# Kernel optimization log

Hardware: AMD Instinct MI355X
Metric: run time of the kernel (lower is better)

## Reference

```python
import jax, jax.numpy as jnp
import numpy as np

NU = 256      # numunits
NH = 32       # torch.split chunk size == head dim in this code
B = 128
S = 256


def _linear_tanh(x, W, b):
    # torch nn.Linear: y = x @ W.T + b, followed by tanh
    return jnp.tanh(x @ W.T + b)


def _split_heads(x):
    # torch.split(x, NH, dim=-1) then cat(dim=0): chunk c occupies rows [c*B, (c+1)*B)
    b, s, d = x.shape
    c = d // NH
    return x.reshape(b, s, c, NH).transpose(2, 0, 1, 3).reshape(c * b, s, NH)


def _merge_heads(x, b):
    # torch.split(x, batchsize, dim=0) then cat(dim=-1): inverse of _split_heads
    cb, s, hd = x.shape
    c = cb // b
    return x.reshape(c, b, s, hd).transpose(1, 2, 0, 3).reshape(b, s, c * hd)


def _attention(Q, K, V):
    d_k = jnp.asarray(K.shape[2], Q.dtype) ** 0.5
    scores = jnp.einsum('nqd,nkd->nqk', Q, K) / d_k
    # NB: original uses F.softmax(scores) with no dim on a 3D tensor ->
    # torch legacy default is dim=0. We reproduce that exactly.
    p_attn = jax.nn.softmax(scores, axis=0)
    return jnp.einsum('nqk,nkd->nqd', p_attn, V)


def setup_inputs() -> dict:
    key = jax.random.key(0)
    ks = jax.random.split(key, 24)
    def w(k):
        return jax.random.normal(k, (NU, NU), dtype=jnp.float32) * 0.02
    def bvec(k):
        return jax.random.normal(k, (NU,), dtype=jnp.float32) * 0.02
    inp = {
        'queries1': jax.random.normal(ks[0], (B, S, NU), dtype=jnp.float32),
        'queries2': jax.random.normal(ks[1], (B, S, NU), dtype=jnp.float32),
        'queries3': jax.random.normal(ks[2], (B, S, NU), dtype=jnp.float32),
        'adj': jax.random.randint(ks[3], (B,), 0, B, dtype=jnp.int64),
        'WQ': w(ks[4]),  'bQ': bvec(ks[5]),
        'WV': w(ks[6]),  'bV': bvec(ks[7]),
        'WQ3': w(ks[8]), 'bQ3': bvec(ks[9]),
        'WK3': w(ks[10]), 'bK3': bvec(ks[11]),
        'WV3': w(ks[12]), 'bV3': bvec(ks[13]),
        'WQ4': w(ks[14]), 'bQ4': bvec(ks[15]),
        'WV4': w(ks[16]), 'bV4': bvec(ks[17]),
        'W5': jax.random.normal(ks[18], (NU, 4 * NU), dtype=jnp.float32) * 0.02,
        'b5': bvec(ks[19]),
    }
    return inp


def reference(queries1, queries2, queries3, adj,
              WQ, bQ, WV, bV, WQ3, bQ3, WK3, bK3, WV3, bV3,
              WQ4, bQ4, WV4, bV4, W5, b5):
    b = queries1.shape[0]
    # per-row batch gather: queries4[i] = queries3[adj[i]]
    queries4 = queries3[adj]

    Q1 = _split_heads(_linear_tanh(queries1, WQ, bQ))
    Q2 = _split_heads(_linear_tanh(queries2, WQ, bQ))
    Q3 = _split_heads(_linear_tanh(queries3, WQ3, bQ3))
    Q4 = _split_heads(_linear_tanh(queries4, WQ4, bQ4))
    K3 = _split_heads(_linear_tanh(queries3, WK3, bK3))
    V1 = _split_heads(_linear_tanh(queries1, WV, bV))
    V2 = _split_heads(_linear_tanh(queries2, WV, bV))
    V3 = _split_heads(_linear_tanh(queries3, WV3, bV3))
    V4 = _split_heads(_linear_tanh(queries4, WV4, bV4))

    o1 = _merge_heads(_attention(Q1, K3, V1), b)
    o2 = _merge_heads(_attention(Q2, K3, V2), b)
    o3 = _merge_heads(_attention(Q3, K3, V3), b)
    o4 = _merge_heads(_attention(Q4, K3, V4), b)

    o5 = jnp.tanh(jnp.concatenate([o1, o2, o3, o4], axis=-1) @ W5.T + b5)
    return (o1, o2, o5, o3)
```

## Files before the change

### kernel.cpp

```cpp
#include <hip/hip_runtime.h>


typedef __attribute__((ext_vector_type(4))) float f32x4;
typedef __attribute__((ext_vector_type(8))) short bf16x8;

#define LOG2E 1.4426950408889634f
#define SM_SCALE (1.4426950408889634f / 5.656854249492381f)

#define CVT_PK(d, lo, hi) \
    asm("v_cvt_pk_bf16_f32 %0, %1, %2" : "=v"(d) : "v"(lo), "v"(hi))
#define SWAP32(x, y) \
    asm("v_permlane32_swap_b32 %0, %1" : "+v"(x), "+v"(y))
#define SWAP16(x, y) \
    asm("v_permlane16_swap_b32 %0, %1" : "+v"(x), "+v"(y))

__device__ __forceinline__ unsigned short f2bf(float x) {
    union { float f; unsigned u; } v; v.f = x;
    unsigned r = v.u + 0x7FFFu + ((v.u >> 16) & 1u);
    return (unsigned short)(r >> 16);
}

__device__ __forceinline__ float fast_tanh(float x) {
    float e = __builtin_amdgcn_exp2f(x * (2.0f * LOG2E));
    return 1.0f - 2.0f * __builtin_amdgcn_rcpf(e + 1.0f);
}

__device__ __forceinline__ f32x4 mfma_bf16(bf16x8 a, bf16x8 b, f32x4 c) {
    return __builtin_amdgcn_mfma_f32_16x16x32_bf16(a, b, c, 0, 0, 0);
}

__global__ __launch_bounds__(256) void k_convert_w(
    const float* w0, const float* w1, const float* w2, const float* w3,
    const float* w4, const float* w5, const float* w6, const float* w7,
    unsigned short* out)
{
    int i = blockIdx.x * 256 + threadIdx.x;
    if (i >= 720896) return;
    float v;
    if (i < 458752) {
        int r = i >> 16, j = i & 65535;
        const float* s =
            (r == 0) ? w0 : (r == 1) ? w1 : (r == 2) ? w2 :
            (r == 3) ? w3 : (r == 4) ? w4 : (r == 5) ? w5 : w6;
        v = s[j];
    } else {
        v = w7[i - 458752];
    }
    out[i] = (short)f2bf(v);
}

__global__ __launch_bounds__(256) void k_convert_x(
    const float* __restrict__ q1, const float* __restrict__ q2,
    const float* __restrict__ q3, unsigned short* __restrict__ Xb)
{
    const int gi = (blockIdx.x * 256 + threadIdx.x) * 8;
    const float* s = (gi < 8388608) ? q1 : (gi < 16777216) ? q2 : q3;
    const int off = gi & 8388607;
    float4 f0 = *(const float4*)(s + off);
    float4 f1 = *(const float4*)(s + off + 4);
    unsigned a0, a1, a2, a3;
    CVT_PK(a0, f0.x, f0.y);
    CVT_PK(a1, f0.z, f0.w);
    CVT_PK(a2, f1.x, f1.y);
    CVT_PK(a3, f1.z, f1.w);
    uint4 pk; pk.x = a0; pk.y = a1; pk.z = a2; pk.w = a3;
    *(uint4*)(Xb + gi) = pk;
}

__global__ __launch_bounds__(512, 4) void k_linear(
    const unsigned short* __restrict__ Xb, const int* __restrict__ adj,
    const unsigned short* __restrict__ wb,
    const float* __restrict__ bQ, const float* __restrict__ bV,
    const float* __restrict__ bQ3, const float* __restrict__ bK3,
    const float* __restrict__ bV3, const float* __restrict__ bQ4,
    const float* __restrict__ bV4,
    unsigned short* __restrict__ lin)
{
    __shared__ __align__(16) short lds[30720];
    const int bid0 = blockIdx.x;
    const int swz = (bid0 & 7) * 320 + (bid0 >> 3);
    const int var = swz >> 9;
    const int rem = swz & 511;
    const int m0 = (rem >> 1) * 128, n0 = (rem & 1) * 128;

    const unsigned short* X = Xb + (size_t)((var == 0) ? 0 : (var == 1) ? 1 : 2) * 8388608;
    const bool gather = (var == 4);
    const int nout = (var == 3) ? 1 : 2;

    int widx0, widx1 = 0, zidx0, zidx1 = 0;
    const float* bp0;
    const float* bp1 = bQ;
    if (var == 0)      { widx0=0; widx1=1; zidx0=0; zidx1=5; bp0=bQ;  bp1=bV;  }
    else if (var == 1) { widx0=0; widx1=1; zidx0=1; zidx1=6; bp0=bQ;  bp1=bV;  }
    else if (var == 2) { widx0=2; widx1=3; zidx0=2; zidx1=4; bp0=bQ3; bp1=bK3; }
    else if (var == 3) { widx0=4;          zidx0=7;          bp0=bV3;          }
    else               { widx0=5; widx1=6; zidx0=3; zidx1=8; bp0=bQ4; bp1=bV4; }

    const int tid = threadIdx.x;
    const int w = tid >> 6, l = tid & 63;
    const int wm = w >> 2, wn = w & 3;
    const int lr = l & 15, lk = (l >> 4) * 8, lq = (l >> 4) * 4;

    const int srow = tid >> 2, scol = (tid & 3) * 8;
    const int gm = m0 + srow;
    const int sm = gather ? (adj[gm >> 8] * 256 + (gm & 255)) : gm;
    const unsigned short* aSrc = X + (size_t)sm * 256 + scol;
    const unsigned short* b0Src = wb + (size_t)widx0 * 65536 + (size_t)(n0 + srow) * 256 + scol;
    const unsigned short* b1Src = wb + (size_t)widx1 * 65536 + (size_t)(n0 + srow) * 256 + scol;

    bf16x8 ar, b0r, b1r;
    f32x4 acc[2][4][2] = {};

    ar = *(const bf16x8*)(aSrc);
    b0r = *(const bf16x8*)(b0Src);
    if (nout == 2) b1r = *(const bf16x8*)(b1Src);
    *(bf16x8*)&lds[srow * 40 + scol] = ar;
    *(bf16x8*)&lds[5120 + srow * 40 + scol] = b0r;
    if (nout == 2) *(bf16x8*)&lds[10240 + srow * 40 + scol] = b1r;
    ar = *(const bf16x8*)(aSrc + 32);
    b0r = *(const bf16x8*)(b0Src + 32);
    if (nout == 2) b1r = *(const bf16x8*)(b1Src + 32);
    __syncthreads();

    for (int st = 0; st < 8; ++st) {
        const int p = st & 1;
        const short* base = lds + p * 15360;
        bf16x8 af[4], bf0[2], bf1[2];
        #pragma unroll
        for (int i = 0; i < 4; ++i)
            af[i] = *(const bf16x8*)&base[(wm * 64 + i * 16 + lr) * 40 + lk];
        #pragma unroll
        for (int j = 0; j < 2; ++j)
            bf0[j] = *(const bf16x8*)&base[5120 + (wn * 32 + j * 16 + lr) * 40 + lk];
        if (nout == 2)
            #pragma unroll
            for (int j = 0; j < 2; ++j)
                bf1[j] = *(const bf16x8*)&base[10240 + (wn * 32 + j * 16 + lr) * 40 + lk];
        #pragma unroll
        for (int i = 0; i < 4; ++i)
            #pragma unroll
            for (int j = 0; j < 2; ++j)
                acc[0][i][j] = mfma_bf16(af[i], bf0[j], acc[0][i][j]);
        if (nout == 2)
            #pragma unroll
            for (int i = 0; i < 4; ++i)
                #pragma unroll
                for (int j = 0; j < 2; ++j)
                    acc[1][i][j] = mfma_bf16(af[i], bf1[j], acc[1][i][j]);
        if (st < 7) {
            short* nbase = lds + (p ^ 1) * 15360;
            *(bf16x8*)&nbase[srow * 40 + scol] = ar;
            *(bf16x8*)&nbase[5120 + srow * 40 + scol] = b0r;
            if (nout == 2) *(bf16x8*)&nbase[10240 + srow * 40 + scol] = b1r;
            if (st < 6) {
                const int ko = (st + 2) * 32;
                ar = *(const bf16x8*)(aSrc + ko);
                b0r = *(const bf16x8*)(b0Src + ko);
                if (nout == 2) b1r = *(const bf16x8*)(b1Src + ko);
            }
        }
        __syncthreads();
    }

    #pragma unroll
    for (int t = 0; t < 2; ++t)
        if (t < nout) {
            const float* bp = t ? bp1 : bp0;
            float bv[2];
            #pragma unroll
            for (int j = 0; j < 2; ++j)
                bv[j] = bp[n0 + wn * 32 + j * 16 + lr];
            #pragma unroll
            for (int i = 0; i < 4; ++i)
                #pragma unroll
                for (int j = 0; j < 2; ++j)
                    #pragma unroll
                    for (int r = 0; r < 4; ++r)
                        lds[(wm * 64 + i * 16 + lq + r) * 136 + wn * 32 + j * 16 + lr] =
                            (short)f2bf(fast_tanh(acc[t][i][j][r] + bv[j]));
            __syncthreads();
            unsigned short* Y = lin + (size_t)(t ? zidx1 : zidx0) * 8388608;
            #pragma unroll
            for (int it2 = 0; it2 < 4; ++it2) {
                const int c = tid + it2 * 512;
                const int row = c >> 4, col8 = (c & 15) * 8;
                *(bf16x8*)(Y + (size_t)(m0 + row) * 256 + n0 + col8) =
                    *(const bf16x8*)&lds[row * 136 + col8];
            }
            __syncthreads();
        }
}

__global__ __launch_bounds__(256) void k_denom(
    const unsigned short* __restrict__ Qa, const unsigned short* __restrict__ Qb2,
    const unsigned short* __restrict__ Qc, const unsigned short* __restrict__ Qd,
    const unsigned short* __restrict__ Kb, float* __restrict__ partialBase)
{
    __shared__ __align__(16) short Qs[2][128 * 40];
    __shared__ __align__(16) short Ks[2][128 * 40];
    const int tid = threadIdx.x, w = tid >> 6, l = tid & 63;
    const int q0 = (blockIdx.x >> 1) * 128, k0 = (blockIdx.x & 1) * 128;
    const int g = blockIdx.y, a = blockIdx.z;
    const unsigned short* Qb = (a == 0) ? Qa : (a == 1) ? Qb2 : (a == 2) ? Qc : Qd;
    float* partial = partialBase + ((size_t)a * 32 + g) * 65536;
    const int lr = l & 15, lk = (l >> 4) * 8, lq = (l >> 4) * 4;

    f32x4 eacc[2][8] = {};
    for (int it = 0; it < 32; it += 2) {
        __syncthreads();
        #pragma unroll
        for (int u = 0; u < 2; ++u) {
            const int n = g * 32 + it + u;
            const int c = n >> 7, b = n & 127;
            const size_t base = (size_t)b * 65536 + (size_t)c * 32;
            for (int ci = tid; ci < 512; ci += 256) {
                int r = ci >> 2, ch = ci & 3;
                *(bf16x8*)&Qs[u][r * 40 + ch * 8] =
                    *(const bf16x8*)(Qb + base + (size_t)(q0 + r) * 256 + ch * 8);
                *(bf16x8*)&Ks[u][r * 40 + ch * 8] =
                    *(const bf16x8*)(Kb + base + (size_t)(k0 + r) * 256 + ch * 8);
            }
        }
        __syncthreads();
        #pragma unroll
        for (int u = 0; u < 2; ++u) {
            bf16x8 aq[2], bk[8];
            #pragma unroll
            for (int i = 0; i < 2; ++i)
                aq[i] = *(const bf16x8*)&Qs[u][(w * 32 + i * 16 + lr) * 40 + lk];
            #pragma unroll
            for (int j = 0; j < 8; ++j)
                bk[j] = *(const bf16x8*)&Ks[u][(j * 16 + lr) * 40 + lk];
            #pragma unroll
            for (int i = 0; i < 2; ++i)
                #pragma unroll
                for (int j = 0; j < 8; ++j) {
                    f32x4 s = mfma_bf16(aq[i], bk[j], (f32x4){0.f, 0.f, 0.f, 0.f});
                    #pragma unroll
                    for (int r = 0; r < 4; ++r)
                        eacc[i][j][r] += __builtin_amdgcn_exp2f(s[r] * SM_SCALE);
                }
        }
    }
    #pragma unroll
    for (int i = 0; i < 2; ++i)
        #pragma unroll
        for (int j = 0; j < 8; ++j)
            #pragma unroll
            for (int r = 0; r < 4; ++r) {
                int q = q0 + w * 32 + i * 16 + lq + r;
                int k = k0 + j * 16 + lr;
                partial[(size_t)q * 256 + k] = eacc[i][j][r];
            }
}

__global__ __launch_bounds__(256) void k_reduce(
    const float* __restrict__ partial, float* __restrict__ dinvP)
{
    int a = blockIdx.y;
    int i = blockIdx.x * 256 + threadIdx.x;
    const float* p = partial + (size_t)a * 32 * 65536 + i;
    float s = 0.f;
    #pragma unroll
    for (int g = 0; g < 32; ++g) s += p[(size_t)g * 65536];
    const int q = i >> 8, k = i & 255;
    const int w_ = q >> 6, iq = (q >> 4) & 3, q16 = q & 15;
    const int kp = k >> 5, j = (k >> 4) & 1, h = (k >> 2) & 3, r = k & 3;
    const int off = (((((((w_ * 8 + kp) * 4 + iq) * 2 + j) * 4 + h) * 16) + q16) * 4) + r;
    dinvP[((size_t)a << 16) + off] = 1.0f / s;
}

__global__ __launch_bounds__(256) void k_attn(
    const unsigned short* __restrict__ Q1, const unsigned short* __restrict__ Q2,
    const unsigned short* __restrict__ Q3, const unsigned short* __restrict__ Q4,
    const unsigned short* __restrict__ Kb,
    const unsigned short* __restrict__ V1, const unsigned short* __restrict__ V2,
    const unsigned short* __restrict__ V3, const unsigned short* __restrict__ V4,
    const float* __restrict__ dinvP,
    float* __restrict__ outBase, unsigned short* __restrict__ ob4)
{
    __shared__ __align__(16) short Vt[32 * 264];
    __shared__ __align__(16) short Ks[256 * 40];
    const int tid = threadIdx.x, w = tid >> 6, l = tid & 63;
    const int bid = blockIdx.x;
    const int swz = (bid & 7) * 512 + (bid >> 3);
    const int a = swz & 3, n = swz >> 2;
    const int c = n >> 7, b = n & 127;
    const int q16 = l & 15, h = l >> 4;
    const size_t base = (size_t)b * 65536 + (size_t)c * 32;

    const unsigned short* Qb = (a == 0) ? Q1 : (a == 1) ? Q2 : (a == 2) ? Q3 : Q4;
    const unsigned short* Vb = (a == 0) ? V1 : (a == 1) ? V2 : (a == 2) ? V3 : V4;
    const f32x4* dw = (const f32x4*)(dinvP + ((size_t)a << 16)) + l + (size_t)w * 4096;
    float* outp = outBase + (size_t)((a == 2) ? 3 : a) * 8388608;

    {
        const unsigned short* vp = Vb + base + (size_t)tid * 256;
        const unsigned short* kp_ = Kb + base + (size_t)tid * 256;
        bf16x8 v0 = *(const bf16x8*)(vp);
        bf16x8 v1 = *(const bf16x8*)(vp + 8);
        bf16x8 v2 = *(const bf16x8*)(vp + 16);
        bf16x8 v3 = *(const bf16x8*)(vp + 24);
        bf16x8 k0 = *(const bf16x8*)(kp_);
        bf16x8 k1 = *(const bf16x8*)(kp_ + 8);
        bf16x8 k2 = *(const bf16x8*)(kp_ + 16);
        bf16x8 k3 = *(const bf16x8*)(kp_ + 24);
        *(bf16x8*)&Ks[tid * 40 + 0]  = k0;
        *(bf16x8*)&Ks[tid * 40 + 8]  = k1;
        *(bf16x8*)&Ks[tid * 40 + 16] = k2;
        *(bf16x8*)&Ks[tid * 40 + 24] = k3;
        #pragma unroll
        for (int e = 0; e < 8; ++e) {
            Vt[(0  + e) * 264 + tid] = v0[e];
            Vt[(8  + e) * 264 + tid] = v1[e];
            Vt[(16 + e) * 264 + tid] = v2[e];
            Vt[(24 + e) * 264 + tid] = v3[e];
        }
    }
    __syncthreads();

    const int q0 = w * 64;
    bf16x8 bq[4];
    #pragma unroll
    for (int i = 0; i < 4; ++i)
        bq[i] = *(const bf16x8*)(Qb + base + (size_t)(q0 + i * 16 + q16) * 256 + h * 8);

    f32x4 dc0 = dw[0];
    f32x4 dc1 = dw[64];

    f32x4 oacc[4][2] = {};
    for (int kp = 0; kp < 8; ++kp) {
        const int kk0 = kp * 32;
        bf16x8 akA = *(const bf16x8*)&Ks[(kk0 + q16) * 40 + h * 8];
        bf16x8 akB = *(const bf16x8*)&Ks[(kk0 + 16 + q16) * 40 + h * 8];
        bf16x8 vb0 = *(const bf16x8*)&Vt[(0  + q16) * 264 + kk0 + h * 8];
        bf16x8 vb1 = *(const bf16x8*)&Vt[(16 + q16) * 264 + kk0 + h * 8];
        #pragma unroll
        for (int i = 0; i < 4; ++i) {
            const int t = kp * 4 + i;
            f32x4 dn0 = dc0, dn1 = dc1;
            if (t < 31) {
                dn0 = dw[(size_t)(t + 1) * 128];
                dn1 = dw[(size_t)(t + 1) * 128 + 64];
            }
            __builtin_amdgcn_s_setprio(1);
            f32x4 s0 = mfma_bf16(akA, bq[i], (f32x4){0.f, 0.f, 0.f, 0.f});
            f32x4 s1 = mfma_bf16(akB, bq[i], (f32x4){0.f, 0.f, 0.f, 0.f});
            __builtin_amdgcn_s_setprio(0);
            float p0 = __builtin_amdgcn_exp2f(s0[0] * SM_SCALE) * dc0[0];
            float p1 = __builtin_amdgcn_exp2f(s0[1] * SM_SCALE) * dc0[1];
            float p2 = __builtin_amdgcn_exp2f(s0[2] * SM_SCALE) * dc0[2];
            float p3 = __builtin_amdgcn_exp2f(s0[3] * SM_SCALE) * dc0[3];
            float p4 = __builtin_amdgcn_exp2f(s1[0] * SM_SCALE) * dc1[0];
            float p5 = __builtin_amdgcn_exp2f(s1[1] * SM_SCALE) * dc1[1];
            float p6 = __builtin_amdgcn_exp2f(s1[2] * SM_SCALE) * dc1[2];
            float p7 = __builtin_amdgcn_exp2f(s1[3] * SM_SCALE) * dc1[3];
            unsigned r0, r1, r2, r3;
            CVT_PK(r0, p0, p1);
            CVT_PK(r1, p2, p3);
            CVT_PK(r2, p4, p5);
            CVT_PK(r3, p6, p7);
            SWAP32(r0, r2); SWAP16(r0, r2);
            SWAP32(r1, r3); SWAP16(r1, r3);
            union { unsigned u[4]; bf16x8 v; } F;
            F.u[0] = r0; F.u[1] = r1; F.u[2] = r2; F.u[3] = r3;
            __builtin_amdgcn_s_setprio(1);
            oacc[i][0] = mfma_bf16(F.v, vb0, oacc[i][0]);
            oacc[i][1] = mfma_bf16(F.v, vb1, oacc[i][1]);
            __builtin_amdgcn_s_setprio(0);
            dc0 = dn0; dc1 = dn1;
        }
    }
    if (a == 3) {
        #pragma unroll
        for (int i = 0; i < 4; ++i)
            #pragma unroll
            for (int d = 0; d < 2; ++d)
                #pragma unroll
                for (int r = 0; r < 4; ++r) {
                    int q = q0 + i * 16 + h * 4 + r;
                    int dc = d * 16 + q16;
                    ob4[(size_t)b * 65536 + (size_t)q * 256 + c * 32 + dc] =
                        f2bf(oacc[i][d][r]);
                }
    } else {
        #pragma unroll
        for (int i = 0; i < 4; ++i)
            #pragma unroll
            for (int d = 0; d < 2; ++d)
                #pragma unroll
                for (int r = 0; r < 4; ++r) {
                    int q = q0 + i * 16 + h * 4 + r;
                    int dc = d * 16 + q16;
                    outp[(size_t)b * 65536 + (size_t)q * 256 + c * 32 + dc] =
                        oacc[i][d][r];
                }
    }
}

__global__ __launch_bounds__(512, 2) void k_final(
    const float* __restrict__ p0, const float* __restrict__ p1,
    const float* __restrict__ p2, const unsigned short* __restrict__ p3,
    const unsigned short* __restrict__ W5b, const float* __restrict__ b5,
    float* __restrict__ out)
{
    __shared__ __align__(16) short As[128 * 72];
    __shared__ __align__(16) short Bs[256 * 72];
    const int tid = threadIdx.x, w = tid >> 6, l = tid & 63;
    const int wm = w >> 2, wn = w & 3;
    const int m0 = blockIdx.x * 128;
    const int lr = l & 15, lk = (l >> 4) * 8, lq = (l >> 4) * 4;

    f32x4 acc[4][4] = {};
    for (int step = 0; step < 16; ++step) {
        const int k0 = step * 64;
        const int kc = k0 & 255;
        __syncthreads();
        if (step < 12) {
            const float* P = (step < 4) ? p0 : (step < 8) ? p1 : p2;
            #pragma unroll
            for (int it = 0; it < 2; ++it) {
                const int cc = tid + it * 512;
                const int row = cc >> 3, ch = cc & 7;
                const float* src = P + (size_t)(m0 + row) * 256 + kc + ch * 8;
                float4 f0 = *(const float4*)src;
                float4 f1 = *(const float4*)(src + 4);
                unsigned a0, a1, a2, a3;
                CVT_PK(a0, f0.x, f0.y);
                CVT_PK(a1, f0.z, f0.w);
                CVT_PK(a2, f1.x, f1.y);
                CVT_PK(a3, f1.z, f1.w);
                uint4 pk; pk.x = a0; pk.y = a1; pk.z = a2; pk.w = a3;
                *(uint4*)&As[row * 72 + ch * 8] = pk;
            }
        } else {
            #pragma unroll
            for (int it = 0; it < 2; ++it) {
                const int cc = tid + it * 512;
                const int row = cc >> 3, ch = cc & 7;
                *(bf16x8*)&As[row * 72 + ch * 8] =
                    *(const bf16x8*)(p3 + (size_t)(m0 + row) * 256 + kc + ch * 8);
            }
        }
        #pragma unroll
        for (int it = 0; it < 4; ++it) {
            const int cc = tid + it * 512;
            const int row = cc >> 3, ch = cc & 7;
            *(bf16x8*)&Bs[row * 72 + ch * 8] =
                *(const bf16x8*)(W5b + (size_t)row * 1024 + k0 + ch * 8);
        }
        __syncthreads();
        #pragma unroll
        for (int kk = 0; kk < 2; ++kk) {
            bf16x8 af[4], bfr[4];
            #pragma unroll
            for (int i = 0; i < 4; ++i)
                af[i] = *(const bf16x8*)&As[(wm * 64 + i * 16 + lr) * 72 + kk * 32 + lk];
            #pragma unroll
            for (int j = 0; j < 4; ++j)
                bfr[j] = *(const bf16x8*)&Bs[(wn * 64 + j * 16 + lr) * 72 + kk * 32 + lk];
            #pragma unroll
            for (int i = 0; i < 4; ++i)
                #pragma unroll
                for (int j = 0; j < 4; ++j)
                    acc[i][j] = mfma_bf16(af[i], bfr[j], acc[i][j]);
        }
    }
    #pragma unroll
    for (int j = 0; j < 4; ++j) {
        int col = wn * 64 + j * 16 + lr;
        float bv = b5[col];
        #pragma unroll
        for (int i = 0; i < 4; ++i) {
            int rowb = m0 + wm * 64 + i * 16 + lq;
            #pragma unroll
            for (int r = 0; r < 4; ++r)
                out[(size_t)(rowb + r) * 256 + col] =
                    fast_tanh(acc[i][j][r] + bv);
        }
    }
}

extern "C" void kernel_launch(void* const* d_in, const int* in_sizes, int n_in,
                              void* d_out, int out_size, void* d_ws, size_t ws_size,
                              hipStream_t stream)
{
    const float* q1  = (const float*)d_in[0];
    const float* q2  = (const float*)d_in[1];
    const float* q3  = (const float*)d_in[2];
    const int*   adj = (const int*)d_in[3];
    const float* WQ  = (const float*)d_in[4];  const float* bQ  = (const float*)d_in[5];
    const float* WV  = (const float*)d_in[6];  const float* bV  = (const float*)d_in[7];
    const float* WQ3 = (const float*)d_in[8];  const float* bQ3 = (const float*)d_in[9];
    const float* WK3 = (const float*)d_in[10]; const float* bK3 = (const float*)d_in[11];
    const float* WV3 = (const float*)d_in[12]; const float* bV3 = (const float*)d_in[13];
    const float* WQ4 = (const float*)d_in[14]; const float* bQ4 = (const float*)d_in[15];
    const float* WV4 = (const float*)d_in[16]; const float* bV4 = (const float*)d_in[17];
    const float* W5  = (const float*)d_in[18]; const float* b5  = (const float*)d_in[19];

    char* ws = (char*)d_ws;
    unsigned short* wb  = (unsigned short*)ws;
    unsigned short* W5b = wb + 458752;
    unsigned short* lin = (unsigned short*)(ws + 1441792);
    unsigned short* Q1 = lin + 0ull * 8388608;
    unsigned short* Q2 = lin + 1ull * 8388608;
    unsigned short* Q3 = lin + 2ull * 8388608;
    unsigned short* Q4 = lin + 3ull * 8388608;
    unsigned short* K3 = lin + 4ull * 8388608;
    unsigned short* V1 = lin + 5ull * 8388608;
    unsigned short* V2 = lin + 6ull * 8388608;
    unsigned short* V3 = lin + 7ull * 8388608;
    unsigned short* V4 = lin + 8ull * 8388608;
    float* partial = (float*)(ws + 152436736);
    float* dinvP   = (float*)(ws + 185991168);
    unsigned short* ob4 = (unsigned short*)(ws + 152436736);

    float* outf = (float*)d_out;
    float* o5p = outf + 2ull * 8388608;
    unsigned short* Xb = (unsigned short*)d_out;

    dim3 blk(256);

    hipLaunchKernelGGL(k_convert_w, dim3(2816), blk, 0, stream,
                       WQ, WV, WQ3, WK3, WV3, WQ4, WV4, W5, wb);
    hipLaunchKernelGGL(k_convert_x, dim3(12288), blk, 0, stream,
                       q1, q2, q3, Xb);

    hipLaunchKernelGGL(k_linear, dim3(2560), dim3(512), 0, stream,
                       Xb, adj, wb,
                       bQ, bV, bQ3, bK3, bV3, bQ4, bV4, lin);

    hipLaunchKernelGGL(k_denom, dim3(4, 32, 4), blk, 0, stream,
                       Q1, Q2, Q3, Q4, K3, partial);
    hipLaunchKernelGGL(k_reduce, dim3(256, 4), blk, 0, stream, partial, dinvP);

    hipLaunchKernelGGL(k_attn, dim3(4096), blk, 0, stream,
                       Q1, Q2, Q3, Q4, K3, V1, V2, V3, V4, dinvP,
                       outf, ob4);

    hipLaunchKernelGGL(k_final, dim3(256), dim3(512), 0, stream,
                       outf, outf + 8388608ull, outf + 3ull * 8388608, ob4,
                       W5b, b5, o5p);
}
```

Before: 305.7 us.

## Use direct global-to-LDS loads in linear GEMM and store bf16 softmax partials

The linear GEMM now stages A and B tiles straight from global memory into LDS using global_load_lds, replacing the register round-trip and the padded LDS layout. The unpadded row stride of 32 shorts may cause LDS bank conflicts on the fragment reads. Separately, the softmax-denominator partial sums are written as packed bf16 vectors in the MFMA register order instead of scattered fp32 stores, and the reduce kernel decodes that layout. This halves partial traffic and makes the stores coalesced, at the cost of bf16 precision in the partial sums before accumulation.

Result: faster. 293.2 us (-4.1%).

```diff
diff --git a/kernel.cpp b/kernel.cpp
--- a/kernel.cpp
+++ b/kernel.cpp
@@ -13,11 +13,19 @@
     asm("v_permlane32_swap_b32 %0, %1" : "+v"(x), "+v"(y))
 #define SWAP16(x, y) \
     asm("v_permlane16_swap_b32 %0, %1" : "+v"(x), "+v"(y))
+#define GLOAD16(g, p) __builtin_amdgcn_global_load_lds( \
+    (const __attribute__((address_space(1))) void*)(g), \
+    (__attribute__((address_space(3))) void*)(p), 16, 0, 0)
 
 __device__ __forceinline__ unsigned short f2bf(float x) {
     union { float f; unsigned u; } v; v.f = x;
     unsigned r = v.u + 0x7FFFu + ((v.u >> 16) & 1u);
     return (unsigned short)(r >> 16);
+}
+
+__device__ __forceinline__ float bf2f(unsigned short x) {
+    union { unsigned u; float f; } v; v.u = ((unsigned)x) << 16;
+    return v.f;
 }
 
 __device__ __forceinline__ float fast_tanh(float x) {
@@ -76,7 +84,7 @@
     const float* __restrict__ bV4,
     unsigned short* __restrict__ lin)
 {
-    __shared__ __align__(16) short lds[30720];
+    __shared__ __align__(16) short lds[24576];
     const int bid0 = blockIdx.x;
     const int swz = (bid0 & 7) * 320 + (bid0 >> 3);
     const int var = swz >> 9;
@@ -101,64 +109,55 @@
     const int wm = w >> 2, wn = w & 3;
     const int lr = l & 15, lk = (l >> 4) * 8, lq = (l >> 4) * 4;
 
-    const int srow = tid >> 2, scol = (tid & 3) * 8;
-    const int gm = m0 + srow;
+    const int rowT = (w << 4) + (l >> 2);
+    const int colT = (l & 3) << 3;
+    const int gm = m0 + rowT;
     const int sm = gather ? (adj[gm >> 8] * 256 + (gm & 255)) : gm;
-    const unsigned short* aSrc = X + (size_t)sm * 256 + scol;
-    const unsigned short* b0Src = wb + (size_t)widx0 * 65536 + (size_t)(n0 + srow) * 256 + scol;
-    const unsigned short* b1Src = wb + (size_t)widx1 * 65536 + (size_t)(n0 + srow) * 256 + scol;
-
-    bf16x8 ar, b0r, b1r;
+    const unsigned short* aG  = X + (size_t)sm * 256 + colT;
+    const unsigned short* b0G = wb + (size_t)widx0 * 65536 + (size_t)(n0 + rowT) * 256 + colT;
+    const unsigned short* b1G = wb + (size_t)widx1 * 65536 + (size_t)(n0 + rowT) * 256 + colT;
+    char* ldsB = (char*)lds;
+    const int wslice = w << 10;
+
     f32x4 acc[2][4][2] = {};
 
-    ar = *(const bf16x8*)(aSrc);
-    b0r = *(const bf16x8*)(b0Src);
-    if (nout == 2) b1r = *(const bf16x8*)(b1Src);
-    *(bf16x8*)&lds[srow * 40 + scol] = ar;
-    *(bf16x8*)&lds[5120 + srow * 40 + scol] = b0r;
-    if (nout == 2) *(bf16x8*)&lds[10240 + srow * 40 + scol] = b1r;
-    ar = *(const bf16x8*)(aSrc + 32);
-    b0r = *(const bf16x8*)(b0Src + 32);
-    if (nout == 2) b1r = *(const bf16x8*)(b1Src + 32);
+    GLOAD16(aG, ldsB + wslice);
+    GLOAD16(b0G, ldsB + 8192 + wslice);
+    if (nout == 2) GLOAD16(b1G, ldsB + 16384 + wslice);
     __syncthreads();
 
     for (int st = 0; st < 8; ++st) {
         const int p = st & 1;
-        const short* base = lds + p * 15360;
-        bf16x8 af[4], bf0[2], bf1[2];
+        if (st < 7) {
+            const int ko = (st + 1) * 32;
+            char* nb = ldsB + (p ^ 1) * 24576;
+            GLOAD16(aG + ko, nb + wslice);
+            GLOAD16(b0G + ko, nb + 8192 + wslice);
+            if (nout == 2) GLOAD16(b1G + ko, nb + 16384 + wslice);
+        }
+        const short* base = lds + p * 12288;
+        bf16x8 af[4], bf0v[2], bf1v[2];
         #pragma unroll
         for (int i = 0; i < 4; ++i)
-            af[i] = *(const bf16x8*)&base[(wm * 64 + i * 16 + lr) * 40 + lk];
+            af[i] = *(const bf16x8*)&base[(wm * 64 + i * 16 + lr) * 32 + lk];
         #pragma unroll
         for (int j = 0; j < 2; ++j)
-            bf0[j] = *(const bf16x8*)&base[5120 + (wn * 32 + j * 16 + lr) * 40 + lk];
+            bf0v[j] = *(const bf16x8*)&base[4096 + (wn * 32 + j * 16 + lr) * 32 + lk];
         if (nout == 2)
             #pragma unroll
             for (int j = 0; j < 2; ++j)
-                bf1[j] = *(const bf16x8*)&base[10240 + (wn * 32 + j * 16 + lr) * 40 + lk];
+                bf1v[j] = *(const bf16x8*)&base[8192 + (wn * 32 + j * 16 + lr) * 32 + lk];
         #pragma unroll
         for (int i = 0; i < 4; ++i)
             #pragma unroll
             for (int j = 0; j < 2; ++j)
-                acc[0][i][j] = mfma_bf16(af[i], bf0[j], acc[0][i][j]);
+                acc[0][i][j] = mfma_bf16(af[i], bf0v[j], acc[0][i][j]);
         if (nout == 2)
             #pragma unroll
             for (int i = 0; i < 4; ++i)
                 #pragma unroll
                 for (int j = 0; j < 2; ++j)
-                    acc[1][i][j] = mfma_bf16(af[i], bf1[j], acc[1][i][j]);
-        if (st < 7) {
-            short* nbase = lds + (p ^ 1) * 15360;
-            *(bf16x8*)&nbase[srow * 40 + scol] = ar;
-            *(bf16x8*)&nbase[5120 + srow * 40 + scol] = b0r;
-            if (nout == 2) *(bf16x8*)&nbase[10240 + srow * 40 + scol] = b1r;
-            if (st < 6) {
-                const int ko = (st + 2) * 32;
-                ar = *(const bf16x8*)(aSrc + ko);
-                b0r = *(const bf16x8*)(b0Src + ko);
-                if (nout == 2) b1r = *(const bf16x8*)(b1Src + ko);
-            }
-        }
+                    acc[1][i][j] = mfma_bf16(af[i], bf1v[j], acc[1][i][j]);
         __syncthreads();
     }
 
@@ -194,7 +193,7 @@
 __global__ __launch_bounds__(256) void k_denom(
     const unsigned short* __restrict__ Qa, const unsigned short* __restrict__ Qb2,
     const unsigned short* __restrict__ Qc, const unsigned short* __restrict__ Qd,
-    const unsigned short* __restrict__ Kb, float* __restrict__ partialBase)
+    const unsigned short* __restrict__ Kb, unsigned short* __restrict__ partial2)
 {
     __shared__ __align__(16) short Qs[2][128 * 40];
     __shared__ __align__(16) short Ks[2][128 * 40];
@@ -202,8 +201,7 @@
     const int q0 = (blockIdx.x >> 1) * 128, k0 = (blockIdx.x & 1) * 128;
     const int g = blockIdx.y, a = blockIdx.z;
     const unsigned short* Qb = (a == 0) ? Qa : (a == 1) ? Qb2 : (a == 2) ? Qc : Qd;
-    float* partial = partialBase + ((size_t)a * 32 + g) * 65536;
-    const int lr = l & 15, lk = (l >> 4) * 8, lq = (l >> 4) * 4;
+    const int lr = l & 15, lk = (l >> 4) * 8;
 
     f32x4 eacc[2][8] = {};
     for (int it = 0; it < 32; it += 2) {
@@ -242,31 +240,36 @@
                 }
         }
     }
+    const size_t pbase = (((size_t)a * 32 + g) << 16) + (size_t)blockIdx.x * 16384;
     #pragma unroll
-    for (int i = 0; i < 2; ++i)
-        #pragma unroll
-        for (int j = 0; j < 8; ++j)
-            #pragma unroll
-            for (int r = 0; r < 4; ++r) {
-                int q = q0 + w * 32 + i * 16 + lq + r;
-                int k = k0 + j * 16 + lr;
-                partial[(size_t)q * 256 + k] = eacc[i][j][r];
-            }
+    for (int cch = 0; cch < 8; ++cch) {
+        const int ii = cch >> 2, jp = (cch & 3) * 2;
+        union { unsigned short s[8]; bf16x8 v; } U;
+        #pragma unroll
+        for (int m = 0; m < 8; ++m)
+            U.s[m] = f2bf(eacc[ii][jp + (m >> 2)][m & 3]);
+        *(bf16x8*)&partial2[pbase + cch * 2048 + tid * 8] = U.v;
+    }
 }
 
 __global__ __launch_bounds__(256) void k_reduce(
-    const float* __restrict__ partial, float* __restrict__ dinvP)
-{
-    int a = blockIdx.y;
-    int i = blockIdx.x * 256 + threadIdx.x;
-    const float* p = partial + (size_t)a * 32 * 65536 + i;
+    const unsigned short* __restrict__ partial2, float* __restrict__ dinvP)
+{
+    const int a = blockIdx.y;
+    const int gi = blockIdx.x * 256 + threadIdx.x;
+    const unsigned short* p = partial2 + (size_t)a * 2097152 + gi;
     float s = 0.f;
     #pragma unroll
-    for (int g = 0; g < 32; ++g) s += p[(size_t)g * 65536];
-    const int q = i >> 8, k = i & 255;
+    for (int g = 0; g < 32; ++g) s += bf2f(p[(size_t)g * 65536]);
+    const int tile = gi >> 14, rem2 = gi & 16383;
+    const int cch = rem2 >> 11, tid2 = (rem2 >> 3) & 255, m = rem2 & 7;
+    const int ii = cch >> 2, j = (cch & 3) * 2 + (m >> 2), r = m & 3;
+    const int w2 = tid2 >> 6, l2 = tid2 & 63;
+    const int q = (tile >> 1) * 128 + w2 * 32 + ii * 16 + ((l2 >> 4) * 4) + r;
+    const int k = (tile & 1) * 128 + j * 16 + (l2 & 15);
     const int w_ = q >> 6, iq = (q >> 4) & 3, q16 = q & 15;
-    const int kp = k >> 5, j = (k >> 4) & 1, h = (k >> 2) & 3, r = k & 3;
-    const int off = (((((((w_ * 8 + kp) * 4 + iq) * 2 + j) * 4 + h) * 16) + q16) * 4) + r;
+    const int kp = k >> 5, jj = (k >> 4) & 1, h = (k >> 2) & 3, rr = k & 3;
+    const int off = (((((((w_ * 8 + kp) * 4 + iq) * 2 + jj) * 4 + h) * 16) + q16) * 4) + rr;
     dinvP[((size_t)a << 16) + off] = 1.0f / s;
 }
 
@@ -511,7 +514,7 @@
     unsigned short* V2 = lin + 6ull * 8388608;
     unsigned short* V3 = lin + 7ull * 8388608;
     unsigned short* V4 = lin + 8ull * 8388608;
-    float* partial = (float*)(ws + 152436736);
+    unsigned short* partial2 = (unsigned short*)(ws + 152436736);
     float* dinvP   = (float*)(ws + 185991168);
     unsigned short* ob4 = (unsigned short*)(ws + 152436736);
 
@@ -531,8 +534,8 @@
                        bQ, bV, bQ3, bK3, bV3, bQ4, bV4, lin);
 
     hipLaunchKernelGGL(k_denom, dim3(4, 32, 4), blk, 0, stream,
-                       Q1, Q2, Q3, Q4, K3, partial);
-    hipLaunchKernelGGL(k_reduce, dim3(256, 4), blk, 0, stream, partial, dinvP);
+                       Q1, Q2, Q3, Q4, K3, partial2);
+    hipLaunchKernelGGL(k_reduce, dim3(256, 4), blk, 0, stream, partial2, dinvP);
 
     hipLaunchKernelGGL(k_attn, dim3(4096), blk, 0, stream,
                        Q1, Q2, Q3, Q4, K3, V1, V2, V3, V4, dinvP,
```
